# Kernel optimization log

Hardware: AMD Instinct MI355X
Metric: run time of the kernel (lower is better)

## Reference

```python
import jax, jax.numpy as jnp
import numpy as np

N, E = 16384, 65536
N2, A2, E2 = 65536, 131072, 262144
N3, A3, E3 = 65536, 196608, 262144
B = 256
F_IN, NI2, NI3 = 16, 64, 64


def setup_inputs() -> dict:
    key = jax.random.key(0)
    ks = iter(jax.random.split(key, 80))
    def rn(shape, s=1.0):
        return jax.random.normal(next(ks), shape, jnp.float32) * s
    def ru(shape):
        return jax.random.uniform(next(ks), shape, dtype=jnp.float32)
    def ri(shape, hi):
        return jax.random.randint(next(ks), shape, 0, hi)
    s = 0.05
    inp = {
        "x": rn((N, F_IN)),
        "edge_index": ri((2, E), N),
        "edge_attr": ru((E, 7)),
        "batch": jnp.sort(ri((N,), B)),
        "assign2_node": ri((A2,), N),
        "assign2_cluster": ri((A2,), N2),
        "iso_type_2": ru((N2, NI2)),
        "edge_index_2": ri((2, E2), N2),
        "batch_2": jnp.sort(ri((N2,), B)),
        "assign3_node": ri((A3,), N),
        "assign3_cluster": ri((A3,), N3),
        "iso_type_3": ru((N3, NI3)),
        "edge_index_3": ri((2, E3), N3),
        "batch_3": jnp.sort(ri((N3,), B)),
    }
    for i, (mi, mo) in enumerate([(F_IN, 32), (32, 64), (64, 64)], start=1):
        inp[f"nn{i}_W1"] = rn((7, 128), s)
        inp[f"nn{i}_b1"] = jnp.zeros((128,), jnp.float32)
        inp[f"nn{i}_W2"] = rn((128, mi * mo), s)
        inp[f"nn{i}_b2"] = jnp.zeros((mi * mo,), jnp.float32)
        inp[f"conv{i}_root"] = rn((mi, mo), s)
        inp[f"conv{i}_bias"] = jnp.zeros((mo,), jnp.float32)
    for i, din in zip([4, 5, 6, 7], [64 + NI2, 64, 64 + NI3, 64]):
        inp[f"conv{i}_Wrel"] = rn((din, 64), s)
        inp[f"conv{i}_Wroot"] = rn((din, 64), s)
        inp[f"conv{i}_bias"] = jnp.zeros((64,), jnp.float32)
    inp["fc1_W"] = rn((384, 64), s); inp["fc1_b"] = jnp.zeros((64,), jnp.float32)
    inp["fc2_W"] = rn((64, 32), s); inp["fc2_b"] = jnp.zeros((32,), jnp.float32)
    inp["fc3_W"] = rn((32, 1), s); inp["fc3_b"] = jnp.zeros((1,), jnp.float32)
    return inp


def nnconv(x, ei, ea, W1, b1, W2, b2, root, bias, mi, mo):
    # edge MLP -> per-edge [mi, mo] weight matrix; message = x_src @ W_e; scatter-add to dst
    h = jax.nn.relu(ea @ W1 + b1) @ W2 + b2          # [E, mi*mo]
    We = h.reshape(-1, mi, mo)
    msg = jnp.einsum('ei,eio->eo', x[ei[0]], We)     # [E, mo]
    agg = jax.ops.segment_sum(msg, ei[1], num_segments=x.shape[0])
    return x @ root + agg + bias


def graphconv(x, ei, Wrel, Wroot, bias):
    agg = jax.ops.segment_sum(x[ei[0]], ei[1], num_segments=x.shape[0])
    return agg @ Wrel + x @ Wroot + bias


def avg_pool_assign(x, node_idx, cluster_idx, num_clusters):
    s = jax.ops.segment_sum(x[node_idx], cluster_idx, num_segments=num_clusters)
    c = jax.ops.segment_sum(jnp.ones((node_idx.shape[0],), x.dtype), cluster_idx, num_segments=num_clusters)
    return s / jnp.clip(c, 1.0)[:, None]


def reference(x, edge_index, edge_attr, batch, assign2_node, assign2_cluster, iso_type_2, edge_index_2, batch_2, assign3_node, assign3_cluster, iso_type_3, edge_index_3, batch_3, nn1_W1, nn1_b1, nn1_W2, nn1_b2, conv1_root, conv1_bias, nn2_W1, nn2_b1, nn2_W2, nn2_b2, conv2_root, conv2_bias, nn3_W1, nn3_b1, nn3_W2, nn3_b2, conv3_root, conv3_bias, conv4_Wrel, conv4_Wroot, conv4_bias, conv5_Wrel, conv5_Wroot, conv5_bias, conv6_Wrel, conv6_Wroot, conv6_bias, conv7_Wrel, conv7_Wroot, conv7_bias, fc1_W, fc1_b, fc2_W, fc2_b, fc3_W, fc3_b):
    elu = jax.nn.elu
    h = elu(nnconv(x, edge_index, edge_attr, nn1_W1, nn1_b1, nn1_W2, nn1_b2, conv1_root, conv1_bias, F_IN, 32))
    h = elu(nnconv(h, edge_index, edge_attr, nn2_W1, nn2_b1, nn2_W2, nn2_b2, conv2_root, conv2_bias, 32, 64))
    h = elu(nnconv(h, edge_index, edge_attr, nn3_W1, nn3_b1, nn3_W2, nn3_b2, conv3_root, conv3_bias, 64, 64))
    x_1 = jax.ops.segment_sum(h, batch, num_segments=B)
    # 2-set level
    h2 = avg_pool_assign(h, assign2_node, assign2_cluster, N2)
    h2 = jnp.concatenate([h2, iso_type_2], axis=1)
    h2 = elu(graphconv(h2, edge_index_2, conv4_Wrel, conv4_Wroot, conv4_bias))
    h2 = elu(graphconv(h2, edge_index_2, conv5_Wrel, conv5_Wroot, conv5_bias))
    x_2 = jax.ops.segment_sum(h2, batch_2, num_segments=B)
    # 3-set level
    h3 = avg_pool_assign(h, assign3_node, assign3_cluster, N3)
    h3 = jnp.concatenate([h3, iso_type_3], axis=1)
    h3 = elu(graphconv(h3, edge_index_3, conv6_Wrel, conv6_Wroot, conv6_bias))
    h3 = elu(graphconv(h3, edge_index_3, conv7_Wrel, conv7_Wroot, conv7_bias))
    x_3 = jax.ops.segment_sum(h3, batch_3, num_segments=B)
    xc = jnp.concatenate([x_1, x_2, x_3], axis=1)
    xc = jnp.concatenate([xc, xc], axis=1)      # [B, 384]
    o = elu(xc @ fc1_W + fc1_b)
    o = elu(o @ fc2_W + fc2_b)
    o = o @ fc3_W + fc3_b
    return o.reshape(-1)
```

## Files before the change

### kernel.cpp

```cpp
#include <hip/hip_runtime.h>
#include <math.h>

#define NN 16384
#define E1N 65536
#define NBATCH 256
#define NC2 65536
#define A2N 131072
#define A3N 196608
#define ELV 262144
#define KH 128
#define OCS 136
#define MNSTR 1092
#define ECAP 96

typedef _Float16 f16;
typedef _Float16 f16x2 __attribute__((ext_vector_type(2)));
typedef _Float16 f16x4 __attribute__((ext_vector_type(4)));
typedef _Float16 f16x8 __attribute__((ext_vector_type(8)));
typedef float    f32x4 __attribute__((ext_vector_type(4)));

__device__ __forceinline__ float elu1(float x){ return x > 0.f ? x : expm1f(x); }

__device__ __forceinline__ float dot2acc(f16x2 a, f16x2 b, float c){
#if __has_builtin(__builtin_amdgcn_fdot2)
  return __builtin_amdgcn_fdot2(a, b, c, false);
#else
  return fmaf((float)a[0], (float)b[0], fmaf((float)a[1], (float)b[1], c));
#endif
}

__global__ __launch_bounds__(256) void k_scan1(const int* __restrict__ deg,
    int* __restrict__ ptr, int* __restrict__ partials){
  __shared__ int buf[256];
  int i = blockIdx.x*256 + threadIdx.x, t = threadIdx.x;
  int v = deg[i];
  buf[t] = v; __syncthreads();
  for (int o = 1; o < 256; o <<= 1){
    int x = (t >= o) ? buf[t-o] : 0;
    __syncthreads(); buf[t] += x; __syncthreads();
  }
  ptr[i] = buf[t] - v;
  if (t == 255) partials[blockIdx.x] = buf[255];
}

__global__ __launch_bounds__(256) void k_scan2seg(int* __restrict__ partials, int nb){
  __shared__ int buf[256];
  int t = threadIdx.x, base = blockIdx.x*nb;
  int v = (t < nb) ? partials[base + t] : 0;
  buf[t] = v; __syncthreads();
  for (int o = 1; o < 256; o <<= 1){
    int x = (t >= o) ? buf[t-o] : 0;
    __syncthreads(); buf[t] += x; __syncthreads();
  }
  if (t < nb) partials[base + t] = buf[t] - v;
}

__global__ __launch_bounds__(256) void k_scan3(const int* __restrict__ partials,
    int* __restrict__ ptr, int* __restrict__ cur){
  int i = blockIdx.x*256 + threadIdx.x;
  int v = ptr[i] + partials[blockIdx.x];
  ptr[i] = v; cur[i] = v;
}

__global__ __launch_bounds__(256) void k_count_edge_dual(const int* __restrict__ ei, int* __restrict__ deg){
  int e = blockIdx.x*256 + threadIdx.x;
  if (e >= E1N) return;
  atomicAdd(&deg[ei[e]], 1);
  atomicAdd(&deg[NN + ei[E1N + e]], 1);
}

__global__ __launch_bounds__(256) void k_fill_edge_dual(const int* __restrict__ ei, int* __restrict__ cur,
    int* __restrict__ eids, int* __restrict__ srcs, int* __restrict__ dpos){
  int e = blockIdx.x*256 + threadIdx.x;
  if (e >= E1N) return;
  int s = ei[e], d = ei[E1N + e];
  int p = atomicAdd(&cur[s], 1);
  eids[p] = e; srcs[p] = s;
  int p2 = atomicAdd(&cur[NN + d], 1);
  dpos[p2] = p;
}

__global__ __launch_bounds__(256) void k_count_assign_dual(const int* __restrict__ a2c,
    const int* __restrict__ a3c, int* __restrict__ ldegA){
  int i = blockIdx.x*256 + threadIdx.x;
  if (i < A2N) atomicAdd(&ldegA[a2c[i]], 1);
  else if (i < A2N + A3N) atomicAdd(&ldegA[NC2 + a3c[i - A2N]], 1);
}

__global__ __launch_bounds__(256) void k_fill_assign_dual(const int* __restrict__ a2n,
    const int* __restrict__ a2c, const int* __restrict__ a3n, const int* __restrict__ a3c,
    int* __restrict__ curA, int* __restrict__ ans2, int* __restrict__ ans3){
  int i = blockIdx.x*256 + threadIdx.x;
  if (i < A2N){
    int p = atomicAdd(&curA[a2c[i]], 1); ans2[p] = a2n[i];
  } else if (i < A2N + A3N){
    int j = i - A2N;
    int p = atomicAdd(&curA[NC2 + a3c[j]], 1); ans3[p] = a3n[j];
  }
}

__global__ __launch_bounds__(256) void k_count_dst_dual(const int* __restrict__ ei2,
    const int* __restrict__ ei3, int* __restrict__ ldegD){
  int i = blockIdx.x*256 + threadIdx.x;
  if (i < ELV) atomicAdd(&ldegD[ei2[ELV + i]], 1);
  else if (i < 2*ELV) atomicAdd(&ldegD[NC2 + ei3[ELV + (i - ELV)]], 1);
}

__global__ __launch_bounds__(256) void k_fill_dst_dual(const int* __restrict__ ei2,
    const int* __restrict__ ei3, int* __restrict__ curD,
    int* __restrict__ dsrc2, int* __restrict__ dsrc3){
  int i = blockIdx.x*256 + threadIdx.x;
  if (i < ELV){
    int p = atomicAdd(&curD[ei2[ELV + i]], 1); dsrc2[p] = ei2[i];
  } else if (i < 2*ELV){
    int j = i - ELV;
    int p = atomicAdd(&curD[NC2 + ei3[ELV + j]], 1); dsrc3[p] = ei3[j];
  }
}

__global__ __launch_bounds__(256) void k_cvt16(const float* __restrict__ v, f16* __restrict__ o, int n){
  int t = blockIdx.x*256 + threadIdx.x;
  if (t < n) o[t] = (f16)v[t];
}

__global__ __launch_bounds__(256) void k_packPrep(const float* __restrict__ root,
    const float* __restrict__ b2, f16* __restrict__ Bp, int mi, int mo, int S, int NB){
  int t = blockIdx.x*256 + threadIdx.x;
  if (t >= NB*S*512) return;
  int j = t & 7, l = (t >> 3) & 63, cs = t >> 9;
  int s = cs % S, c = cs / S;
  int k_in = s*32 + ((l>>4)<<3) + j;
  int n = c*16 + (l & 15);
  float v = 0.f;
  if (k_in < mi) v = (n < mo) ? root[k_in*mo + n] : b2[k_in*mo + (n - mo)];
  Bp[t] = (f16)v;
}

template<int MI, int S, int NB, int MO>
__global__ __launch_bounds__(256) void k_prep_mfma(const f16* __restrict__ A,
    const f16* __restrict__ Bp, const float* __restrict__ bias,
    float* __restrict__ prep, float* __restrict__ bterm){
  int l = threadIdx.x & 63, w = threadIdx.x >> 6;
  int r0 = blockIdx.x*64 + w*16;
  const f16* arow = A + (size_t)(r0 + (l & 15))*MI;
  f16x8 a[S];
  #pragma unroll
  for (int s=0;s<S;s++){
    int koff = s*32 + ((l>>4)<<3);
    if (koff < MI) a[s] = *(const f16x8*)(arow + koff);
    else           a[s] = (f16x8){0,0,0,0,0,0,0,0};
  }
  #pragma unroll
  for (int c=0;c<NB;c++){
    f32x4 acc = (f32x4){0.f,0.f,0.f,0.f};
    #pragma unroll
    for (int s=0;s<S;s++){
      f16x8 b = *(const f16x8*)(Bp + ((size_t)(c*S + s)*64 + l)*8);
      acc = __builtin_amdgcn_mfma_f32_16x16x32_f16(a[s], b, acc, 0, 0, 0);
    }
    int col = c*16 + (l & 15);
    #pragma unroll
    for (int r=0;r<4;r++){
      int row = r0 + ((l>>4)<<2) + r;
      if (col < MO) prep[(size_t)row*MO + col] = acc[r] + bias[col];
      else          bterm[(size_t)row*MO + (col - MO)] = acc[r];
    }
  }
}

__global__ __launch_bounds__(256) void k_w2pack_full(const float* __restrict__ W2,
    f16* __restrict__ Bp, int mi, int mo, int S){
  int t = blockIdx.x*256 + threadIdx.x;
  if (t >= mo*8*S*512) return;
  int j = t & 7, l = (t >> 3) & 63, cs = t >> 9;
  int s = cs % S, q = cs / S;
  int oc = q >> 3;
  int k  = (q & 7)*16 + (l & 15);
  int i  = s*32 + ((l>>4)<<3) + j;
  float v = (i < mi) ? W2[(size_t)k*mi*mo + (size_t)i*mo + oc] : 0.f;
  Bp[t] = (f16)v;
}

template<int MI, int S, int MO>
__global__ __launch_bounds__(256) void k_nnconv_fused5(const f16* __restrict__ xin16,
    const f16* __restrict__ W2p,
    const int* __restrict__ rowptr, const int* __restrict__ rowend,
    const int* __restrict__ srcs, const int* __restrict__ eids,
    const float* __restrict__ ea, const float* __restrict__ W1,
    const float* __restrict__ b1,
    const float* __restrict__ bterm, f16* __restrict__ msg16){
  __shared__ __align__(16) f16   M[16*MNSTR];
  __shared__ __align__(16) f16   hb[ECAP*OCS];
  __shared__ __align__(16) float eas[ECAP*8];
  __shared__ float bt[16*MO];
  int t = threadIdx.x, l = t & 63, w = t >> 6;
  int n0 = blockIdx.x*16;
  int estart = rowptr[n0], eend = rowend[n0+15];
  if (estart >= eend) return;
  for (int idx = t; idx < 16*MO; idx += 256) bt[idx] = bterm[(size_t)n0*MO + idx];
  const f16* arow = xin16 + (size_t)(n0 + (l&15))*MI;
  f16x8 a[S];
  #pragma unroll
  for (int s=0;s<S;s++){
    int koff = s*32 + ((l>>4)<<3);
    if (koff < MI) a[s] = *(const f16x8*)(arow + koff);
    else           a[s] = (f16x8){0,0,0,0,0,0,0,0};
  }
  const int NCHUNK = MO/8;
  int oc = t & 7, eslot = t >> 3;
  for (int ebase = estart; ebase < eend; ebase += ECAP){
    int ecnt = eend - ebase; if (ecnt > ECAP) ecnt = ECAP;
    for (int idx = t; idx < ecnt*8; idx += 256){
      int e_ = idx >> 3, i = idx & 7;
      eas[idx] = (i < 7) ? ea[(size_t)eids[ebase + e_]*7 + i] : 0.f;
    }
    __syncthreads();
    for (int idx = t; idx < ecnt*32; idx += 256){
      int e_ = idx >> 5, p = idx & 31;
      int k0 = p*4;
      const float* xr = &eas[e_*8];
      float4 acc4 = *(const float4*)(b1 + k0);
      #pragma unroll
      for (int i=0;i<7;i++){
        float xv = xr[i];
        float4 wv = *(const float4*)(W1 + i*KH + k0);
        acc4.x = fmaf(xv, wv.x, acc4.x);
        acc4.y = fmaf(xv, wv.y, acc4.y);
        acc4.z = fmaf(xv, wv.z, acc4.z);
        acc4.w = fmaf(xv, wv.w, acc4.w);
      }
      f16x4 hv = { (f16)fmaxf(acc4.x,0.f), (f16)fmaxf(acc4.y,0.f),
                   (f16)fmaxf(acc4.z,0.f), (f16)fmaxf(acc4.w,0.f) };
      *(f16x4*)&hb[e_*OCS + k0] = hv;
    }
    __syncthreads();
    for (int c = 0; c < NCHUNK; c++){
      #pragma unroll
      for (int tt = 0; tt < 16; tt++){
        int q = c*64 + w*16 + tt;
        f32x4 acc = (f32x4){0.f,0.f,0.f,0.f};
        #pragma unroll
        for (int s=0;s<S;s++){
          f16x8 b = *(const f16x8*)(W2p + ((size_t)(q*S + s)*64 + l)*8);
          acc = __builtin_amdgcn_mfma_f32_16x16x32_f16(a[s], b, acc, 0, 0, 0);
        }
        int ocl = w*2 + (tt>>3);
        int kpos = (tt&7)*16 + (l & 15);
        f16* mp = &M[ocl*OCS + kpos];
        #pragma unroll
        for (int r=0;r<4;r++)
          mp[(size_t)(((l>>4)<<2) + r)*MNSTR] = (f16)acc[r];
      }
      __syncthreads();
      #pragma unroll
      for (int r2 = 0; r2 < ECAP/32; r2++){
        int ee = r2*32 + eslot;
        if (ee < ecnt){
          int e = ebase + ee;
          int s_ = srcs[e];
          int ln = s_ - n0;
          float acc = bt[ln*MO + c*8 + oc];
          const f16* mrow = &M[(size_t)ln*MNSTR + oc*OCS];
          const f16* hrow = &hb[ee*OCS];
          #pragma unroll 4
          for (int kk=0; kk<16; kk++){
            f16x8 h8 = *(const f16x8*)(hrow + kk*8);
            f16x4 m0 = *(const f16x4*)(mrow + kk*8);
            f16x4 m1 = *(const f16x4*)(mrow + kk*8 + 4);
            acc = dot2acc((f16x2){h8[0],h8[1]}, (f16x2){m0[0],m0[1]}, acc);
            acc = dot2acc((f16x2){h8[2],h8[3]}, (f16x2){m0[2],m0[3]}, acc);
            acc = dot2acc((f16x2){h8[4],h8[5]}, (f16x2){m1[0],m1[1]}, acc);
            acc = dot2acc((f16x2){h8[6],h8[7]}, (f16x2){m1[2],m1[3]}, acc);
          }
          msg16[(size_t)e*MO + c*8 + oc] = (f16)acc;
        }
      }
      __syncthreads();
    }
  }
}

template<int MO>
__global__ __launch_bounds__(256) void k_msg_gather(const int* __restrict__ dptr,
    const int* __restrict__ dend, const int* __restrict__ dpos,
    const f16* __restrict__ msg, const float* __restrict__ prep,
    f16* __restrict__ out16){
  int t = threadIdx.x, l = t & 63, w = t >> 6;
  int n, o;
  if (MO == 64){ n = blockIdx.x*4 + w; o = l; }
  else         { n = blockIdx.x*8 + w*2 + (l>>5); o = l & 31; }
  int st = dptr[n], en = dend[n];
  float acc = prep[(size_t)n*MO + o];
  int p = st;
  for (; p+1 < en; p += 2){
    int q0 = dpos[p], q1 = dpos[p+1];
    acc += (float)msg[(size_t)q0*MO + o];
    acc += (float)msg[(size_t)q1*MO + o];
  }
  if (p < en) acc += (float)msg[(size_t)dpos[p]*MO + o];
  out16[(size_t)n*MO + o] = (f16)elu1(acc);
}

__global__ __launch_bounds__(256) void k_pool_gather_dual(const int* __restrict__ aptr,
    const int* __restrict__ aend, const int* __restrict__ ans2, const int* __restrict__ ans3,
    const f16* __restrict__ h, const float* __restrict__ iso2, const float* __restrict__ iso3,
    f16* __restrict__ h16){
  int l = threadIdx.x & 63, w = threadIdx.x >> 6;
  int cg = blockIdx.x*4 + w;
  int lvl = cg >= NC2;
  int c = cg - lvl*NC2;
  const int* ans = lvl ? ans3 : ans2;
  const float* iso = lvl ? iso3 : iso2;
  int st = aptr[cg], en = aend[cg];
  float acc = 0.f;
  int e = st;
  for (; e+1 < en; e += 2){
    int n0 = ans[e], n1 = ans[e+1];
    acc += (float)h[(size_t)n0*64 + l];
    acc += (float)h[(size_t)n1*64 + l];
  }
  if (e < en) acc += (float)h[(size_t)ans[e]*64 + l];
  int cnt = en - st;
  float val = (cnt > 0) ? acc / (float)cnt : 0.f;
  h16[(size_t)cg*128 + l] = (f16)val;
  h16[(size_t)cg*128 + 64 + l] = (f16)iso[(size_t)c*64 + l];
}

#define BP_O4 0
#define BP_O5 16384
#define BP_O6 24576
#define BP_O7 40960
__global__ __launch_bounds__(256) void k_packB_all(
    const float* __restrict__ W4r, const float* __restrict__ W4o,
    const float* __restrict__ W5r, const float* __restrict__ W5o,
    const float* __restrict__ W6r, const float* __restrict__ W6o,
    const float* __restrict__ W7r, const float* __restrict__ W7o,
    f16* __restrict__ Bp){
  int t = blockIdx.x*256 + threadIdx.x;
  const float *Wrel, *Wroot; int S, base;
  if      (t < BP_O5){ Wrel=W4r; Wroot=W4o; S=4; base=BP_O4; }
  else if (t < BP_O6){ Wrel=W5r; Wroot=W5o; S=2; base=BP_O5; }
  else if (t < BP_O7){ Wrel=W6r; Wroot=W6o; S=4; base=BP_O6; }
  else if (t < 49152){ Wrel=W7r; Wroot=W7o; S=2; base=BP_O7; }
  else return;
  int u = t - base;
  int j = u & 7, l = (u >> 3) & 63, cs = u >> 9;
  int s = cs % S, c = cs / S;
  int k = s*32 + ((l>>4)<<3) + j;
  int n = (c<<4) + (l & 15);
  float v = (n < 64) ? Wrel[k*64 + n] : Wroot[k*64 + (n - 64)];
  Bp[t] = (f16)v;
}

template<int S>
__global__ __launch_bounds__(256) void k_gc_mfma_dual(const f16* __restrict__ Abase,
    const f16* __restrict__ Bp, int bpo2, int bpo3,
    const float* __restrict__ bias2, const float* __restrict__ bias3,
    f16* __restrict__ y16, f16* __restrict__ rbuf16){
  const int half = NC2/64;
  int lvl = blockIdx.x >= half;
  int bloc = blockIdx.x - lvl*half;
  const f16* A = Abase + (size_t)lvl*NC2*(S*32);
  const f16* B = Bp + (lvl ? bpo3 : bpo2);
  const float* bias = lvl ? bias3 : bias2;
  f16* y  = y16 + (size_t)lvl*NC2*64;
  f16* rb = rbuf16 + (size_t)lvl*NC2*64;
  int l = threadIdx.x & 63, w = threadIdx.x >> 6;
  int r0 = bloc*64 + w*16;
  const f16* arow = A + (size_t)(r0 + (l & 15))*(S*32);
  f16x8 a[S];
  #pragma unroll
  for (int s=0;s<S;s++) a[s] = *(const f16x8*)(arow + s*32 + ((l>>4)<<3));
  f32x4 acc[8];
  #pragma unroll
  for (int c=0;c<8;c++) acc[c] = (f32x4){0.f,0.f,0.f,0.f};
  #pragma unroll
  for (int c=0;c<8;c++){
    #pragma unroll
    for (int s=0;s<S;s++){
      f16x8 b = *(const f16x8*)(B + ((size_t)(c*S + s)*64 + l)*8);
      acc[c] = __builtin_amdgcn_mfma_f32_16x16x32_f16(a[s], b, acc[c], 0, 0, 0);
    }
  }
  #pragma unroll
  for (int c=0;c<8;c++){
    int col = c*16 + (l & 15);
    #pragma unroll
    for (int r=0;r<4;r++){
      int row = r0 + ((l>>4)<<2) + r;
      if (col < 64) y[(size_t)row*64 + col] = (f16)acc[c][r];
      else          rb[(size_t)row*64 + (col-64)] = (f16)(acc[c][r] + bias[col-64]);
    }
  }
}

__global__ __launch_bounds__(256) void k_gc_gather_dual(const int* __restrict__ dptrD,
    const int* __restrict__ dcurD, const int* __restrict__ dsrc2, const int* __restrict__ dsrc3,
    const f16* __restrict__ y16, const f16* __restrict__ rbuf16,
    f16* __restrict__ obase){
  int l = threadIdx.x & 63, w = threadIdx.x >> 6;
  int ng = blockIdx.x*4 + w;
  int lvl = ng >= NC2;
  int n = ng - lvl*NC2;
  const int* dsrc = lvl ? dsrc3 : dsrc2;
  const f16* y  = y16 + (size_t)lvl*NC2*64;
  const f16* rb = rbuf16 + (size_t)lvl*NC2*64;
  f16* o = obase + (size_t)lvl*NC2*64;
  int st = dptrD[ng], en = dcurD[ng];
  float acc = (float)rb[(size_t)n*64 + l];
  int e = st;
  for (; e+1 < en; e += 2){
    int s0 = dsrc[e], s1 = dsrc[e+1];
    acc += (float)y[(size_t)s0*64 + l];
    acc += (float)y[(size_t)s1*64 + l];
  }
  if (e < en) acc += (float)y[(size_t)dsrc[e]*64 + l];
  o[(size_t)n*64 + l] = (f16)elu1(acc);
}

__device__ __forceinline__ int lowerb(const int* __restrict__ a, int n, int key){
  int lo = 0, hi = n;
  while (lo < hi){ int m = (lo + hi) >> 1; if (a[m] < key) lo = m + 1; else hi = m; }
  return lo;
}

__global__ __launch_bounds__(256) void k_batchsum3(const int* __restrict__ b1,
    const int* __restrict__ b2, const int* __restrict__ b3,
    const f16* __restrict__ s1, const f16* __restrict__ s2, const f16* __restrict__ s3,
    float* __restrict__ x123){
  __shared__ float red[4][64];
  int seg = blockIdx.x >> 8, b = blockIdx.x & 255;
  const int* batch = (seg==0) ? b1 : ((seg==1) ? b2 : b3);
  const f16* src   = (seg==0) ? s1 : ((seg==1) ? s2 : s3);
  int nn = (seg==0) ? NN : NC2;
  int lo = lowerb(batch, nn, b);
  int hi = lowerb(batch, nn, b+1);
  int col = threadIdx.x & 63, wq = threadIdx.x >> 6;
  float acc = 0.f;
  for (int n = lo + wq; n < hi; n += 4) acc += (float)src[(size_t)n*64 + col];
  red[wq][col] = acc;
  __syncthreads();
  if (threadIdx.x < 64){
    float s = red[0][threadIdx.x] + red[1][threadIdx.x] + red[2][threadIdx.x] + red[3][threadIdx.x];
    x123[b*192 + seg*64 + threadIdx.x] = s;
  }
}

__global__ __launch_bounds__(256) void k_fc1(const float* __restrict__ x123,
    const float* __restrict__ W, const float* __restrict__ b, float* __restrict__ t1){
  int t = blockIdx.x*256 + threadIdx.x;
  if (t >= NBATCH*64) return;
  int bb = t >> 6, o = t & 63;
  const float* xr = x123 + bb*192;
  float acc = b[o];
  for (int j=0;j<192;j++) acc = fmaf(xr[j], W[j*64+o] + W[(192+j)*64+o], acc);
  t1[t] = elu1(acc);
}

__global__ __launch_bounds__(256) void k_fc2(const float* __restrict__ t1,
    const float* __restrict__ W, const float* __restrict__ b, float* __restrict__ t2){
  int t = blockIdx.x*256 + threadIdx.x;
  if (t >= NBATCH*32) return;
  int bb = t >> 5, o = t & 31;
  float acc = b[o];
  for (int j=0;j<64;j++) acc = fmaf(t1[bb*64+j], W[j*32+o], acc);
  t2[t] = elu1(acc);
}

__global__ __launch_bounds__(256) void k_fc3(const float* __restrict__ t2,
    const float* __restrict__ W, const float* __restrict__ b, float* __restrict__ out){
  int t = blockIdx.x*256 + threadIdx.x;
  if (t >= NBATCH) return;
  float acc = b[0];
  for (int j=0;j<32;j++) acc = fmaf(t2[t*32+j], W[j], acc);
  out[t] = acc;
}

static inline int cdiv(long long a, int b){ return (int)((a + b - 1) / b); }

extern "C" void kernel_launch(void* const* d_in, const int* in_sizes, int n_in,
                              void* d_out, int out_size, void* d_ws, size_t ws_size,
                              hipStream_t stream) {
  const float* x0    = (const float*)d_in[0];
  const int*   ei    = (const int*)d_in[1];
  const float* ea    = (const float*)d_in[2];
  const int*   batch = (const int*)d_in[3];
  const int*   a2n   = (const int*)d_in[4];
  const int*   a2c   = (const int*)d_in[5];
  const float* iso2  = (const float*)d_in[6];
  const int*   ei2   = (const int*)d_in[7];
  const int*   b2arr = (const int*)d_in[8];
  const int*   a3n   = (const int*)d_in[9];
  const int*   a3c   = (const int*)d_in[10];
  const float* iso3  = (const float*)d_in[11];
  const int*   ei3   = (const int*)d_in[12];
  const int*   b3arr = (const int*)d_in[13];
  const float* nnp[3][6];
  for (int c=0;c<3;c++) for (int p=0;p<6;p++) nnp[c][p] = (const float*)d_in[14 + 6*c + p];
  const float* c4W[3]; const float* c5W[3]; const float* c6W[3]; const float* c7W[3];
  for (int p=0;p<3;p++){ c4W[p]=(const float*)d_in[32+p]; c5W[p]=(const float*)d_in[35+p];
                         c6W[p]=(const float*)d_in[38+p]; c7W[p]=(const float*)d_in[41+p]; }
  const float* fc1W=(const float*)d_in[44]; const float* fc1b=(const float*)d_in[45];
  const float* fc2W=(const float*)d_in[46]; const float* fc2b=(const float*)d_in[47];
  const float* fc3W=(const float*)d_in[48]; const float* fc3b=(const float*)d_in[49];
  float* outp = (float*)d_out;

  char* ws = (char*)d_ws; size_t off = 0;
  auto alloc = [&](size_t bytes)->void*{ void* p = ws + off; off += (bytes + 255) & ~(size_t)255; return p; };
  const size_t SZ_R0 = (size_t)92*1024*1024;
  char* r0 = (char*)alloc(SZ_R0);
  f16*   W2p   = (f16*)r0;
  f16*   prepB = (f16*)(r0 + 2*1024*1024);
  float* bterm = (float*)(r0 + 2*1024*1024 + 64*1024);
  float* prep  = (float*)(r0 + 2*1024*1024 + 64*1024 + (size_t)NN*64*4);
  f16*   msg16 = (f16*)  (r0 + 2*1024*1024 + 64*1024 + (size_t)NN*64*8);
  size_t o2 = 0;
  auto a2 = [&](size_t bytes)->char*{ char* p = r0 + o2; o2 += (bytes + 255) & ~(size_t)255; return p; };
  f16*   h16   = (f16*)  a2((size_t)2*NC2*128*2);
  f16*   y16   = (f16*)  a2((size_t)2*NC2*64*2);
  f16*   rbuf16= (f16*)  a2((size_t)2*NC2*64*2);
  f16*   g16   = (f16*)  a2((size_t)2*NC2*64*2);
  f16*   BpGc  = (f16*)  a2((size_t)49152*2);
  int*   ldegA = (int*)  a2((size_t)4*NC2*4);
  int*   ldegD = ldegA + 2*NC2;
  int*   ptrA  = (int*)  a2((size_t)2*NC2*4);
  int*   curA  = (int*)  a2((size_t)2*NC2*4);
  int*   ptrD  = (int*)  a2((size_t)2*NC2*4);
  int*   curD  = (int*)  a2((size_t)2*NC2*4);
  int*   ans2  = (int*)  a2((size_t)A2N*4);
  int*   ans3  = (int*)  a2((size_t)A3N*4);
  int*   dsrc2 = (int*)  a2((size_t)ELV*4);
  int*   dsrc3 = (int*)  a2((size_t)ELV*4);
  f16*   fin2  = h16;
  f16*   fin3  = h16 + (size_t)NC2*64;
  f16*   x016  = (f16*)  alloc((size_t)NN*16*2);
  f16*   hA16  = (f16*)  alloc((size_t)NN*32*2);
  f16*   hB16  = (f16*)  alloc((size_t)NN*64*2);
  f16*   hC16  = (f16*)  alloc((size_t)NN*64*2);
  int*   deg1  = (int*)  alloc((size_t)2*NN*4);
  int*   ptr1  = (int*)  alloc((size_t)2*NN*4);
  int*   cur1  = (int*)  alloc((size_t)2*NN*4);
  int*   eids  = (int*)  alloc((size_t)E1N*4);
  int*   srcs  = (int*)  alloc((size_t)E1N*4);
  int*   dpos  = (int*)  alloc((size_t)E1N*4);
  int*   parts = (int*)  alloc((size_t)512*4);
  float* x123  = (float*)alloc((size_t)NBATCH*192*4);
  float* t1    = (float*)alloc((size_t)NBATCH*64*4);
  float* t2    = (float*)alloc((size_t)NBATCH*32*4);
  (void)ws_size; (void)n_in; (void)in_sizes; (void)out_size;

  auto scan = [&](const int* dg, int totalN, int segs, int* ptr, int* cur){
    int nb = totalN/256/segs;
    k_scan1<<<totalN/256,256,0,stream>>>(dg, ptr, parts);
    k_scan2seg<<<segs,256,0,stream>>>(parts, nb);
    k_scan3<<<totalN/256,256,0,stream>>>(parts, ptr, cur);
  };

  hipMemsetAsync(deg1, 0, (size_t)2*NN*4, stream);
  k_count_edge_dual<<<cdiv(E1N,256),256,0,stream>>>(ei, deg1);
  scan(deg1, 2*NN, 2, ptr1, cur1);
  k_fill_edge_dual<<<cdiv(E1N,256),256,0,stream>>>(ei, cur1, eids, srcs, dpos);
  k_cvt16<<<cdiv((long long)NN*16,256),256,0,stream>>>(x0, x016, NN*16);

  auto run_nnconv = [&](const f16* xin16, int mi, int mo,
                        const float* const* P, f16* out16){
    const float* W1=P[0]; const float* b1=P[1]; const float* W2=P[2];
    const float* b2=P[3]; const float* root=P[4]; const float* bias=P[5];
    const int S = (mi > 32) ? 2 : 1;
    const int NB = (2*mo)/16;
    k_packPrep<<<cdiv((long long)NB*S*512,256),256,0,stream>>>(root, b2, prepB, mi, mo, S, NB);
    if (mi==16)      k_prep_mfma<16,1,4,32><<<NN/64,256,0,stream>>>(xin16, prepB, bias, prep, bterm);
    else if (mi==32) k_prep_mfma<32,1,8,64><<<NN/64,256,0,stream>>>(xin16, prepB, bias, prep, bterm);
    else             k_prep_mfma<64,2,8,64><<<NN/64,256,0,stream>>>(xin16, prepB, bias, prep, bterm);
    k_w2pack_full<<<cdiv((long long)mo*8*S*512,256),256,0,stream>>>(W2, W2p, mi, mo, S);
    if (mi==16)      k_nnconv_fused5<16,1,32><<<NN/16,256,0,stream>>>(xin16, W2p, ptr1, cur1, srcs, eids, ea, W1, b1, bterm, msg16);
    else if (mi==32) k_nnconv_fused5<32,1,64><<<NN/16,256,0,stream>>>(xin16, W2p, ptr1, cur1, srcs, eids, ea, W1, b1, bterm, msg16);
    else             k_nnconv_fused5<64,2,64><<<NN/16,256,0,stream>>>(xin16, W2p, ptr1, cur1, srcs, eids, ea, W1, b1, bterm, msg16);
    if (mo==32) k_msg_gather<32><<<NN/8,256,0,stream>>>(ptr1+NN, cur1+NN, dpos, msg16, prep, out16);
    else        k_msg_gather<64><<<NN/4,256,0,stream>>>(ptr1+NN, cur1+NN, dpos, msg16, prep, out16);
  };
  run_nnconv(x016, 16, 32, nnp[0], hA16);
  run_nnconv(hA16, 32, 64, nnp[1], hB16);
  run_nnconv(hB16, 64, 64, nnp[2], hC16);

  hipMemsetAsync(ldegA, 0, (size_t)4*NC2*4, stream);
  k_count_assign_dual<<<cdiv((long long)(A2N+A3N),256),256,0,stream>>>(a2c, a3c, ldegA);
  scan(ldegA, 2*NC2, 2, ptrA, curA);
  k_fill_assign_dual<<<cdiv((long long)(A2N+A3N),256),256,0,stream>>>(a2n, a2c, a3n, a3c, curA, ans2, ans3);
  k_count_dst_dual<<<cdiv((long long)2*ELV,256),256,0,stream>>>(ei2, ei3, ldegD);
  scan(ldegD, 2*NC2, 2, ptrD, curD);
  k_fill_dst_dual<<<cdiv((long long)2*ELV,256),256,0,stream>>>(ei2, ei3, curD, dsrc2, dsrc3);

  k_pool_gather_dual<<<2*NC2/4,256,0,stream>>>(ptrA, curA, ans2, ans3, hC16, iso2, iso3, h16);
  k_packB_all<<<cdiv(49152,256),256,0,stream>>>(c4W[0], c4W[1], c5W[0], c5W[1],
                                                c6W[0], c6W[1], c7W[0], c7W[1], BpGc);
  k_gc_mfma_dual<4><<<2*NC2/64,256,0,stream>>>(h16, BpGc, BP_O4, BP_O6, c4W[2], c6W[2], y16, rbuf16);
  k_gc_gather_dual<<<2*NC2/4,256,0,stream>>>(ptrD, curD, dsrc2, dsrc3, y16, rbuf16, g16);
  k_gc_mfma_dual<2><<<2*NC2/64,256,0,stream>>>(g16, BpGc, BP_O5, BP_O7, c5W[2], c7W[2], y16, rbuf16);
  k_gc_gather_dual<<<2*NC2/4,256,0,stream>>>(ptrD, curD, dsrc2, dsrc3, y16, rbuf16, fin2);

  k_batchsum3<<<3*NBATCH,256,0,stream>>>(batch, b2arr, b3arr, hC16, fin2, fin3, x123);
  k_fc1<<<cdiv((long long)NBATCH*64,256),256,0,stream>>>(x123, fc1W, fc1b, t1);
  k_fc2<<<cdiv((long long)NBATCH*32,256),256,0,stream>>>(t1, fc2W, fc2b, t2);
  k_fc3<<<cdiv(NBATCH,256),256,0,stream>>>(t2, fc3W, fc3b, outp);
}
```

Baseline: 747.2 us.

## Keep edge-MLP hidden activations in registers and split K across lanes

Measured after the change: 1.041 ms. 1.39x slower.

```diff
diff --git a/kernel.cpp b/kernel.cpp
--- a/kernel.cpp
+++ b/kernel.cpp
@@ -182,7 +182,7 @@
 }
 
 template<int MI, int S, int MO>
-__global__ __launch_bounds__(256) void k_nnconv_fused5(const f16* __restrict__ xin16,
+__global__ __launch_bounds__(256,3) void k_nnconv_fused6(const f16* __restrict__ xin16,
     const f16* __restrict__ W2p,
     const int* __restrict__ rowptr, const int* __restrict__ rowend,
     const int* __restrict__ srcs, const int* __restrict__ eids,
@@ -190,7 +190,6 @@
     const float* __restrict__ b1,
     const float* __restrict__ bterm, f16* __restrict__ msg16){
   __shared__ __align__(16) f16   M[16*MNSTR];
-  __shared__ __align__(16) f16   hb[ECAP*OCS];
   __shared__ __align__(16) float eas[ECAP*8];
   __shared__ float bt[16*MO];
   int t = threadIdx.x, l = t & 63, w = t >> 6;
@@ -207,7 +206,8 @@
     else           a[s] = (f16x8){0,0,0,0,0,0,0,0};
   }
   const int NCHUNK = MO/8;
-  int oc = t & 7, eslot = t >> 3;
+  const int NR = ECAP/32;
+  int eslot = t >> 3, kg = t & 7;
   for (int ebase = estart; ebase < eend; ebase += ECAP){
     int ecnt = eend - ebase; if (ecnt > ECAP) ecnt = ECAP;
     for (int idx = t; idx < ecnt*8; idx += 256){
@@ -215,25 +215,39 @@
       eas[idx] = (i < 7) ? ea[(size_t)eids[ebase + e_]*7 + i] : 0.f;
     }
     __syncthreads();
-    for (int idx = t; idx < ecnt*32; idx += 256){
-      int e_ = idx >> 5, p = idx & 31;
-      int k0 = p*4;
-      const float* xr = &eas[e_*8];
-      float4 acc4 = *(const float4*)(b1 + k0);
-      #pragma unroll
-      for (int i=0;i<7;i++){
-        float xv = xr[i];
-        float4 wv = *(const float4*)(W1 + i*KH + k0);
-        acc4.x = fmaf(xv, wv.x, acc4.x);
-        acc4.y = fmaf(xv, wv.y, acc4.y);
-        acc4.z = fmaf(xv, wv.z, acc4.z);
-        acc4.w = fmaf(xv, wv.w, acc4.w);
+    f16x8 hreg[NR][2];
+    int   sreg[NR];
+    #pragma unroll
+    for (int r2 = 0; r2 < NR; r2++){
+      int ee = r2*32 + eslot;
+      if (ee < ecnt){
+        sreg[r2] = srcs[ebase + ee];
+        const float* xr = &eas[ee*8];
+        float xv[7];
+        #pragma unroll
+        for (int i=0;i<7;i++) xv[i] = xr[i];
+        float hacc[16];
+        #pragma unroll
+        for (int j4=0;j4<4;j4++){
+          int k0 = kg*16 + j4*4;
+          float4 acc4 = *(const float4*)(b1 + k0);
+          #pragma unroll
+          for (int i=0;i<7;i++){
+            float4 wv = *(const float4*)(W1 + i*KH + k0);
+            acc4.x = fmaf(xv[i], wv.x, acc4.x);
+            acc4.y = fmaf(xv[i], wv.y, acc4.y);
+            acc4.z = fmaf(xv[i], wv.z, acc4.z);
+            acc4.w = fmaf(xv[i], wv.w, acc4.w);
+          }
+          hacc[j4*4+0] = fmaxf(acc4.x, 0.f);
+          hacc[j4*4+1] = fmaxf(acc4.y, 0.f);
+          hacc[j4*4+2] = fmaxf(acc4.z, 0.f);
+          hacc[j4*4+3] = fmaxf(acc4.w, 0.f);
+        }
+        #pragma unroll
+        for (int j=0;j<8;j++){ hreg[r2][0][j] = (f16)hacc[j]; hreg[r2][1][j] = (f16)hacc[8+j]; }
       }
-      f16x4 hv = { (f16)fmaxf(acc4.x,0.f), (f16)fmaxf(acc4.y,0.f),
-                   (f16)fmaxf(acc4.z,0.f), (f16)fmaxf(acc4.w,0.f) };
-      *(f16x4*)&hb[e_*OCS + k0] = hv;
     }
-    __syncthreads();
     for (int c = 0; c < NCHUNK; c++){
       #pragma unroll
       for (int tt = 0; tt < 16; tt++){
@@ -253,26 +267,37 @@
       }
       __syncthreads();
       #pragma unroll
-      for (int r2 = 0; r2 < ECAP/32; r2++){
+      for (int r2 = 0; r2 < NR; r2++){
         int ee = r2*32 + eslot;
         if (ee < ecnt){
           int e = ebase + ee;
-          int s_ = srcs[e];
-          int ln = s_ - n0;
-          float acc = bt[ln*MO + c*8 + oc];
-          const f16* mrow = &M[(size_t)ln*MNSTR + oc*OCS];
-          const f16* hrow = &hb[ee*OCS];
-          #pragma unroll 4
-          for (int kk=0; kk<16; kk++){
-            f16x8 h8 = *(const f16x8*)(hrow + kk*8);
-            f16x4 m0 = *(const f16x4*)(mrow + kk*8);
-            f16x4 m1 = *(const f16x4*)(mrow + kk*8 + 4);
-            acc = dot2acc((f16x2){h8[0],h8[1]}, (f16x2){m0[0],m0[1]}, acc);
-            acc = dot2acc((f16x2){h8[2],h8[3]}, (f16x2){m0[2],m0[3]}, acc);
-            acc = dot2acc((f16x2){h8[4],h8[5]}, (f16x2){m1[0],m1[1]}, acc);
-            acc = dot2acc((f16x2){h8[6],h8[7]}, (f16x2){m1[2],m1[3]}, acc);
+          int ln = sreg[r2] - n0;
+          const f16* mrow = &M[(size_t)ln*MNSTR + kg*16];
+          f16x8 h0 = hreg[r2][0], h1 = hreg[r2][1];
+          float p[8];
+          #pragma unroll
+          for (int oc=0;oc<8;oc++){
+            f16x8 m0 = *(const f16x8*)(mrow + oc*OCS);
+            f16x8 m1 = *(const f16x8*)(mrow + oc*OCS + 8);
+            float acc = 0.f;
+            #pragma unroll
+            for (int j=0;j<4;j++){
+              acc = dot2acc((f16x2){h0[2*j],h0[2*j+1]}, (f16x2){m0[2*j],m0[2*j+1]}, acc);
+              acc = dot2acc((f16x2){h1[2*j],h1[2*j+1]}, (f16x2){m1[2*j],m1[2*j+1]}, acc);
+            }
+            p[oc] = acc;
           }
-          msg16[(size_t)e*MO + c*8 + oc] = (f16)acc;
+          #pragma unroll
+          for (int m = 1; m < 8; m <<= 1){
+            #pragma unroll
+            for (int oc=0;oc<8;oc++) p[oc] += __shfl_xor(p[oc], m, 64);
+          }
+          if (kg == 0){
+            f16x8 out;
+            #pragma unroll
+            for (int oc=0;oc<8;oc++) out[oc] = (f16)(p[oc] + bt[ln*MO + c*8 + oc]);
+            *(f16x8*)&msg16[(size_t)e*MO + c*8] = out;
+          }
         }
       }
       __syncthreads();
@@ -573,9 +598,9 @@
     else if (mi==32) k_prep_mfma<32,1,8,64><<<NN/64,256,0,stream>>>(xin16, prepB, bias, prep, bterm);
     else             k_prep_mfma<64,2,8,64><<<NN/64,256,0,stream>>>(xin16, prepB, bias, prep, bterm);
     k_w2pack_full<<<cdiv((long long)mo*8*S*512,256),256,0,stream>>>(W2, W2p, mi, mo, S);
-    if (mi==16)      k_nnconv_fused5<16,1,32><<<NN/16,256,0,stream>>>(xin16, W2p, ptr1, cur1, srcs, eids, ea, W1, b1, bterm, msg16);
-    else if (mi==32) k_nnconv_fused5<32,1,64><<<NN/16,256,0,stream>>>(xin16, W2p, ptr1, cur1, srcs, eids, ea, W1, b1, bterm, msg16);
-    else             k_nnconv_fused5<64,2,64><<<NN/16,256,0,stream>>>(xin16, W2p, ptr1, cur1, srcs, eids, ea, W1, b1, bterm, msg16);
+    if (mi==16)      k_nnconv_fused6<16,1,32><<<NN/16,256,0,stream>>>(xin16, W2p, ptr1, cur1, srcs, eids, ea, W1, b1, bterm, msg16);
+    else if (mi==32) k_nnconv_fused6<32,1,64><<<NN/16,256,0,stream>>>(xin16, W2p, ptr1, cur1, srcs, eids, ea, W1, b1, bterm, msg16);
+    else             k_nnconv_fused6<64,2,64><<<NN/16,256,0,stream>>>(xin16, W2p, ptr1, cur1, srcs, eids, ea, W1, b1, bterm, msg16);
     if (mo==32) k_msg_gather<32><<<NN/8,256,0,stream>>>(ptr1+NN, cur1+NN, dpos, msg16, prep, out16);
     else        k_msg_gather<64><<<NN/4,256,0,stream>>>(ptr1+NN, cur1+NN, dpos, msg16, prep, out16);
   };
```
